# Kernel optimization log

Measured on AMD Instinct MI355X. Metric: run time of the kernel, lower is better.

Reference implementation:

```python
import jax, jax.numpy as jnp
from jax import lax
import numpy as np

ALPHA = 1.702  # GLU sigmoid scale
LIMIT = 7.0    # swiglu_limit


def _moe_forward(hidden_states, topk_weights, topk_ids, gate_up_proj, gate_up_proj_bias, down_proj, down_proj_bias):
    T, H = hidden_states.shape
    E = gate_up_proj.shape[0]
    K = topk_ids.shape[1]
    flat = jnp.ravel(topk_ids)                               # [T*K]
    sorted_sel = jnp.argsort(flat, stable=True)              # dispatch permutation
    sorted_token = sorted_sel // K                           # source token per slot
    sorted_inputs = jnp.take(hidden_states, sorted_token, axis=0)  # [T*K, H]
    expert_ids = jnp.take(flat, sorted_sel, axis=0)          # [T*K]
    group_sizes = jnp.bincount(flat, length=E).astype(jnp.int32)
    # grouped GEMM 1: [T*K,H] x [E,H,2F] -> [T*K,2F]
    gate_up = lax.ragged_dot(sorted_inputs, gate_up_proj, group_sizes)
    gate_up = gate_up + gate_up_proj_bias[expert_ids]
    gate = jnp.minimum(gate_up[..., ::2], LIMIT)
    up = jnp.clip(gate_up[..., 1::2], -LIMIT, LIMIT)
    glu = gate * jax.nn.sigmoid(gate * ALPHA)
    intermediate = (up + 1.0) * glu                          # [T*K, F]
    # grouped GEMM 2: [T*K,F] x [E,F,H] -> [T*K,H]
    out = lax.ragged_dot(intermediate, down_proj, group_sizes)
    out = out + down_proj_bias[expert_ids]
    unsort = jnp.argsort(sorted_sel, stable=True)
    out = jnp.take(out, unsort, axis=0).reshape(T, K, H).astype(jnp.float32)
    combined = jnp.einsum('tkh,tk->th', out, topk_weights.astype(jnp.float32))
    return combined.astype(hidden_states.dtype)


def setup_inputs() -> dict:
    key = jax.random.key(0)
    ks = jax.random.split(key, 7)
    T, H, E, F, K = 16384, 1024, 16, 2048, 2
    scale = 0.02
    hidden_states = jax.random.normal(ks[0], (T, H), jnp.float32)
    w = jax.random.uniform(ks[1], (T, K), jnp.float32) + 1e-3
    topk_weights = w / jnp.sum(w, axis=-1, keepdims=True)
    topk_ids = jax.random.randint(ks[2], (T, K), 0, E, dtype=jnp.int32)
    gate_up_proj = jax.random.normal(ks[3], (E, H, 2 * F), jnp.float32) * scale
    gate_up_proj_bias = jax.random.normal(ks[4], (E, 2 * F), jnp.float32) * scale
    down_proj = jax.random.normal(ks[5], (E, F, H), jnp.float32) * scale
    down_proj_bias = jax.random.normal(ks[6], (E, H), jnp.float32) * scale
    return {"hidden_states": hidden_states, "topk_weights": topk_weights, "topk_ids": topk_ids,
            "gate_up_proj": gate_up_proj, "gate_up_proj_bias": gate_up_proj_bias,
            "down_proj": down_proj, "down_proj_bias": down_proj_bias}


def reference(hidden_states, topk_weights, topk_ids, gate_up_proj, gate_up_proj_bias, down_proj, down_proj_bias):
    return _moe_forward(hidden_states, topk_weights, topk_ids, gate_up_proj, gate_up_proj_bias, down_proj, down_proj_bias)
```

## Files before the change

### kernel.cpp

```cpp
#include <hip/hip_runtime.h>
#include <hip/hip_bf16.h>

typedef unsigned short ushort_t;
typedef __attribute__((ext_vector_type(8))) short bf16x8;
typedef __attribute__((ext_vector_type(4))) float f32x4;

#define T_TOK 16384
#define H_DIM 1024
#define E_NUM 16
#define F_DIM 2048
#define TK    32768
#define MAX_TILES 272

static __device__ __forceinline__ unsigned short f2bf(float f) {
    unsigned int u = __builtin_bit_cast(unsigned int, f);
    unsigned int r = (u + 0x7fffu + ((u >> 16) & 1u)) >> 16;
    return (unsigned short)r;
}

#define GLOAD_LDS16(gp, lp) \
    __builtin_amdgcn_global_load_lds( \
        (const __attribute__((address_space(1))) unsigned int*)(gp), \
        (__attribute__((address_space(3))) unsigned int*)(lp), 16, 0, 0)

__global__ void k_hist(const int* __restrict__ ids, int* __restrict__ meta) {
    __shared__ int h[E_NUM];
    int tid = threadIdx.x;
    if (tid < E_NUM) h[tid] = 0;
    __syncthreads();
    int i = blockIdx.x * 256 + tid;
    atomicAdd(&h[ids[i]], 1);
    __syncthreads();
    if (tid < E_NUM) atomicAdd(&meta[tid], h[tid]);
}

__global__ void k_scan(int* __restrict__ meta) {
    if (threadIdx.x != 0) return;
    int off = 0;
    for (int e = 0; e < E_NUM; ++e) {
        meta[16 + e] = off;
        meta[40 + e] = off;
        off += meta[e];
    }
    meta[32] = off;
    int nt = 0;
    for (int e = 0; e < E_NUM; ++e) {
        int s = meta[16 + e], en = s + meta[e];
        for (int r = s; r < en; r += 128) {
            meta[128 + nt * 3 + 0] = r;
            meta[128 + nt * 3 + 1] = en;
            meta[128 + nt * 3 + 2] = e;
            ++nt;
        }
    }
    meta[64] = nt;
}

__global__ void k_scatter(const int* __restrict__ ids, int* __restrict__ meta,
                          int* __restrict__ row2slot, int* __restrict__ pos2slot) {
    int i = blockIdx.x * 256 + threadIdx.x;
    int e = ids[i];
    int p = atomicAdd(&meta[40 + e], 1);
    row2slot[p] = i;
    pos2slot[i] = p;
}

__global__ void k_gather(const float* __restrict__ hs, const int* __restrict__ row2slot,
                         ushort_t* __restrict__ A1) {
    int r = blockIdx.x;
    int tid = threadIdx.x;
    int tok = row2slot[r] >> 1;
    float4 v = *(const float4*)(hs + (size_t)tok * H_DIM + tid * 4);
    ushort4 o;
    o.x = f2bf(v.x); o.y = f2bf(v.y); o.z = f2bf(v.z); o.w = f2bf(v.w);
    *(ushort4*)(A1 + (size_t)r * H_DIM + tid * 4) = o;
}

__global__ void k_w1conv(const float* __restrict__ gu, ushort_t* __restrict__ w1g,
                         ushort_t* __restrict__ w1u) {
    __shared__ float t[64][65];
    int b = blockIdx.x;
    int nt = b & 63;
    int kt = (b >> 6) & 15;
    int e  = b >> 10;
    int n0 = nt * 64, k0 = kt * 64;
    const float* src = gu + ((size_t)e * H_DIM + k0) * (2 * F_DIM) + n0;
    for (int i = threadIdx.x; i < 64 * 64; i += 256) {
        int kr = i >> 6, nc = i & 63;
        t[kr][nc] = src[(size_t)kr * (2 * F_DIM) + nc];
    }
    __syncthreads();
    ushort_t* dg = w1g + ((size_t)e * F_DIM + (n0 >> 1)) * H_DIM + k0;
    ushort_t* du = w1u + ((size_t)e * F_DIM + (n0 >> 1)) * H_DIM + k0;
    for (int i = threadIdx.x; i < 32 * 64; i += 256) {
        int jl = i >> 6, kc = i & 63;
        dg[(size_t)jl * H_DIM + kc] = f2bf(t[kc][2 * jl]);
        du[(size_t)jl * H_DIM + kc] = f2bf(t[kc][2 * jl + 1]);
    }
}

__global__ void k_w2conv(const float* __restrict__ dp, ushort_t* __restrict__ w2t) {
    __shared__ float t[64][65];
    int b = blockIdx.x;
    int ht = b & 15;
    int ft = (b >> 4) & 31;
    int e  = b >> 9;
    int h0 = ht * 64, f0 = ft * 64;
    const float* src = dp + ((size_t)e * F_DIM + f0) * H_DIM + h0;
    for (int i = threadIdx.x; i < 64 * 64; i += 256) {
        int fr = i >> 6, hc = i & 63;
        t[fr][hc] = src[(size_t)fr * H_DIM + hc];
    }
    __syncthreads();
    ushort_t* d = w2t + ((size_t)e * H_DIM + h0) * F_DIM + f0;
    for (int i = threadIdx.x; i < 64 * 64; i += 256) {
        int hl = i >> 6, fc = i & 63;
        d[(size_t)hl * F_DIM + fc] = f2bf(t[fc][hl]);
    }
}

__global__ __launch_bounds__(256) void k_gemm1(
    const ushort_t* __restrict__ A1, const ushort_t* __restrict__ W1g,
    const ushort_t* __restrict__ W1u, const float* __restrict__ bias,
    ushort_t* __restrict__ inter, const int* __restrict__ meta) {
    int nt = meta[64];
    int slot = blockIdx.y;
    if (slot >= nt) return;
    int row0    = meta[128 + slot * 3 + 0];
    int row_end = meta[128 + slot * 3 + 1];
    int e       = meta[128 + slot * 3 + 2];
    int j0 = blockIdx.x * 64;
    int tid = threadIdx.x, lane = tid & 63, wid = tid >> 6;
    int wm = wid & 1, wj = wid >> 1;
    int lm = lane & 15, lq = lane >> 4;
    __shared__ char smem[32 * 1024];

    f32x4 accg[4][2], accu[4][2];
#pragma unroll
    for (int mi = 0; mi < 4; ++mi)
#pragma unroll
        for (int ji = 0; ji < 2; ++ji) {
            accg[mi][ji] = (f32x4){0.f, 0.f, 0.f, 0.f};
            accu[mi][ji] = (f32x4){0.f, 0.f, 0.f, 0.f};
        }

    for (int kt = 0; kt < 16; ++kt) {
        int kb = kt * 64;
        __syncthreads();
#pragma unroll
        for (int f = 0; f < 8; ++f) {
            int fr = wid * 8 + f;
            const ushort_t* gp;
            if (fr < 16) {
                int mi = fr >> 1, kc = fr & 1;
                int r = row0 + mi * 16 + lm;
                if (r > TK - 1) r = TK - 1;
                gp = A1 + ((size_t)r << 10) + kb + kc * 32 + lq * 8;
            } else if (fr < 24) {
                int g2 = fr - 16; int ji = g2 >> 1, kc = g2 & 1;
                int j = j0 + ji * 16 + lm;
                gp = W1g + (((size_t)(e * F_DIM + j)) << 10) + kb + kc * 32 + lq * 8;
            } else {
                int g2 = fr - 24; int ji = g2 >> 1, kc = g2 & 1;
                int j = j0 + ji * 16 + lm;
                gp = W1u + (((size_t)(e * F_DIM + j)) << 10) + kb + kc * 32 + lq * 8;
            }
            GLOAD_LDS16(gp, smem + fr * 1024);
        }
        __syncthreads();
#pragma unroll
        for (int kc = 0; kc < 2; ++kc) {
            bf16x8 af[4], bg[2], bu[2];
#pragma unroll
            for (int mi = 0; mi < 4; ++mi)
                af[mi] = *(const bf16x8*)(smem + ((wm * 4 + mi) * 2 + kc) * 1024 + lane * 16);
#pragma unroll
            for (int ji = 0; ji < 2; ++ji) {
                bg[ji] = *(const bf16x8*)(smem + 16 * 1024 + ((wj * 2 + ji) * 2 + kc) * 1024 + lane * 16);
                bu[ji] = *(const bf16x8*)(smem + 24 * 1024 + ((wj * 2 + ji) * 2 + kc) * 1024 + lane * 16);
            }
#pragma unroll
            for (int mi = 0; mi < 4; ++mi)
#pragma unroll
                for (int ji = 0; ji < 2; ++ji) {
                    accg[mi][ji] = __builtin_amdgcn_mfma_f32_16x16x32_bf16(af[mi], bg[ji], accg[mi][ji], 0, 0, 0);
                    accu[mi][ji] = __builtin_amdgcn_mfma_f32_16x16x32_bf16(af[mi], bu[ji], accu[mi][ji], 0, 0, 0);
                }
        }
    }
#pragma unroll
    for (int mi = 0; mi < 4; ++mi)
#pragma unroll
        for (int ji = 0; ji < 2; ++ji) {
            int j = j0 + (wj * 2 + ji) * 16 + lm;
            float bgv = bias[e * (2 * F_DIM) + 2 * j];
            float buv = bias[e * (2 * F_DIM) + 2 * j + 1];
#pragma unroll
            for (int r = 0; r < 4; ++r) {
                int row = row0 + wm * 64 + mi * 16 + lq * 4 + r;
                if (row < row_end) {
                    float g = accg[mi][ji][r] + bgv;
                    g = fminf(g, 7.0f);
                    float u = accu[mi][ji][r] + buv;
                    u = fminf(fmaxf(u, -7.0f), 7.0f);
                    float glu = g / (1.0f + __expf(-1.702f * g));
                    inter[((size_t)row << 11) + j] = f2bf((u + 1.0f) * glu);
                }
            }
        }
}

__global__ __launch_bounds__(256) void k_gemm2(
    const ushort_t* __restrict__ Ain, const ushort_t* __restrict__ W2t,
    float* __restrict__ out2, const int* __restrict__ meta) {
    int nt = meta[64];
    int slot = blockIdx.y;
    if (slot >= nt) return;
    int row0    = meta[128 + slot * 3 + 0];
    int row_end = meta[128 + slot * 3 + 1];
    int e       = meta[128 + slot * 3 + 2];
    int n0 = blockIdx.x * 128;
    int tid = threadIdx.x, lane = tid & 63, wid = tid >> 6;
    int wm = wid & 1, wn = wid >> 1;
    int lm = lane & 15, lq = lane >> 4;
    __shared__ char smem[32 * 1024];

    f32x4 acc[4][4];
#pragma unroll
    for (int mi = 0; mi < 4; ++mi)
#pragma unroll
        for (int ni = 0; ni < 4; ++ni) acc[mi][ni] = (f32x4){0.f, 0.f, 0.f, 0.f};

    for (int kt = 0; kt < 32; ++kt) {
        int kb = kt * 64;
        __syncthreads();
#pragma unroll
        for (int f = 0; f < 8; ++f) {
            int fr = wid * 8 + f;
            const ushort_t* gp;
            if (fr < 16) {
                int mi = fr >> 1, kc = fr & 1;
                int r = row0 + mi * 16 + lm;
                if (r > TK - 1) r = TK - 1;
                gp = Ain + ((size_t)r << 11) + kb + kc * 32 + lq * 8;
            } else {
                int g2 = fr - 16; int ni = g2 >> 1, kc = g2 & 1;
                int n = n0 + ni * 16 + lm;
                gp = W2t + (((size_t)(e * H_DIM + n)) << 11) + kb + kc * 32 + lq * 8;
            }
            GLOAD_LDS16(gp, smem + fr * 1024);
        }
        __syncthreads();
#pragma unroll
        for (int kc = 0; kc < 2; ++kc) {
            bf16x8 af[4], bf[4];
#pragma unroll
            for (int mi = 0; mi < 4; ++mi)
                af[mi] = *(const bf16x8*)(smem + ((wm * 4 + mi) * 2 + kc) * 1024 + lane * 16);
#pragma unroll
            for (int ni = 0; ni < 4; ++ni)
                bf[ni] = *(const bf16x8*)(smem + 16 * 1024 + ((wn * 4 + ni) * 2 + kc) * 1024 + lane * 16);
#pragma unroll
            for (int mi = 0; mi < 4; ++mi)
#pragma unroll
                for (int ni = 0; ni < 4; ++ni)
                    acc[mi][ni] = __builtin_amdgcn_mfma_f32_16x16x32_bf16(af[mi], bf[ni], acc[mi][ni], 0, 0, 0);
        }
    }
#pragma unroll
    for (int mi = 0; mi < 4; ++mi)
#pragma unroll
        for (int ni = 0; ni < 4; ++ni) {
            int n = n0 + (wn * 4 + ni) * 16 + lm;
#pragma unroll
            for (int r = 0; r < 4; ++r) {
                int row = row0 + wm * 64 + mi * 16 + lq * 4 + r;
                if (row < row_end)
                    out2[((size_t)row << 10) + n] = acc[mi][ni][r];
            }
        }
}

__global__ void k_combine(const float* __restrict__ out2, const float* __restrict__ tw,
                          const int* __restrict__ ids, const float* __restrict__ db,
                          const int* __restrict__ pos2slot, float* __restrict__ out) {
    int t = blockIdx.x;
    int tid = threadIdx.x;
    float w0 = tw[2 * t], w1 = tw[2 * t + 1];
    int p0 = pos2slot[2 * t], p1 = pos2slot[2 * t + 1];
    int e0 = ids[2 * t], e1 = ids[2 * t + 1];
    int h = tid * 4;
    float4 a0 = *(const float4*)(out2 + ((size_t)p0 << 10) + h);
    float4 a1 = *(const float4*)(out2 + ((size_t)p1 << 10) + h);
    float4 b0 = *(const float4*)(db + ((size_t)e0 << 10) + h);
    float4 b1 = *(const float4*)(db + ((size_t)e1 << 10) + h);
    float4 o;
    o.x = w0 * (a0.x + b0.x) + w1 * (a1.x + b1.x);
    o.y = w0 * (a0.y + b0.y) + w1 * (a1.y + b1.y);
    o.z = w0 * (a0.z + b0.z) + w1 * (a1.z + b1.z);
    o.w = w0 * (a0.w + b0.w) + w1 * (a1.w + b1.w);
    *(float4*)(out + (size_t)t * H_DIM + h) = o;
}

#define WS_META      0
#define WS_R2S       8192
#define WS_P2S       139264
#define WS_A1        270336
#define WS_W1G       67379200
#define WS_W1U       134488064
#define WS_W2T       201596928
#define WS_INTER     268705792

extern "C" void kernel_launch(void* const* d_in, const int* in_sizes, int n_in,
                              void* d_out, int out_size, void* d_ws, size_t ws_size,
                              hipStream_t stream) {
    (void)in_sizes; (void)n_in; (void)out_size; (void)ws_size;
    const float* hs  = (const float*)d_in[0];
    const float* tw  = (const float*)d_in[1];
    const int*   ids = (const int*)d_in[2];
    const float* gup = (const float*)d_in[3];
    const float* gub = (const float*)d_in[4];
    const float* dp  = (const float*)d_in[5];
    const float* dpb = (const float*)d_in[6];
    float* out = (float*)d_out;
    char* ws = (char*)d_ws;

    int* meta          = (int*)(ws + WS_META);
    int* row2slot      = (int*)(ws + WS_R2S);
    int* pos2slot      = (int*)(ws + WS_P2S);
    ushort_t* A1       = (ushort_t*)(ws + WS_A1);
    ushort_t* W1g      = (ushort_t*)(ws + WS_W1G);
    ushort_t* W1u      = (ushort_t*)(ws + WS_W1U);
    ushort_t* W2t      = (ushort_t*)(ws + WS_W2T);
    ushort_t* inter    = (ushort_t*)(ws + WS_INTER);
    float* out2        = (float*)(ws + WS_W1G);

    hipMemsetAsync(meta, 0, 8192, stream);
    k_hist<<<128, 256, 0, stream>>>(ids, meta);
    k_scan<<<1, 64, 0, stream>>>(meta);
    k_scatter<<<128, 256, 0, stream>>>(ids, meta, row2slot, pos2slot);
    k_gather<<<TK, 256, 0, stream>>>(hs, row2slot, A1);
    k_w1conv<<<16384, 256, 0, stream>>>(gup, W1g, W1u);
    k_w2conv<<<8192, 256, 0, stream>>>(dp, W2t);
    k_gemm1<<<dim3(32, MAX_TILES), 256, 0, stream>>>(A1, W1g, W1u, gub, inter, meta);
    k_gemm2<<<dim3(8, MAX_TILES), 256, 0, stream>>>(inter, W2t, out2, meta);
    k_combine<<<T_TOK, 256, 0, stream>>>(out2, tw, ids, dpb, pos2slot, out);
}
```

Before: 1.621 ms.

## Double-buffer LDS tiles in both grouped GEMM kernels to overlap loads with MFMA

```diff
diff --git a/kernel.cpp b/kernel.cpp
--- a/kernel.cpp
+++ b/kernel.cpp
@@ -133,7 +133,35 @@
     int tid = threadIdx.x, lane = tid & 63, wid = tid >> 6;
     int wm = wid & 1, wj = wid >> 1;
     int lm = lane & 15, lq = lane >> 4;
-    __shared__ char smem[32 * 1024];
+    __shared__ char smem[2][32 * 1024];
+
+    const ushort_t* gbase[8];
+#pragma unroll
+    for (int f = 0; f < 8; ++f) {
+        int fr = wid * 8 + f;
+        const ushort_t* gp;
+        if (fr < 16) {
+            int mi = fr >> 1, kc = fr & 1;
+            int r = row0 + mi * 16 + lm;
+            if (r > TK - 1) r = TK - 1;
+            gp = A1 + ((size_t)r << 10) + kc * 32 + lq * 8;
+        } else if (fr < 24) {
+            int g2 = fr - 16; int ji = g2 >> 1, kc = g2 & 1;
+            int j = j0 + ji * 16 + lm;
+            gp = W1g + (((size_t)(e * F_DIM + j)) << 10) + kc * 32 + lq * 8;
+        } else {
+            int g2 = fr - 24; int ji = g2 >> 1, kc = g2 & 1;
+            int j = j0 + ji * 16 + lm;
+            gp = W1u + (((size_t)(e * F_DIM + j)) << 10) + kc * 32 + lq * 8;
+        }
+        gbase[f] = gp;
+    }
+
+    auto stage = [&](int buf, int kb) {
+#pragma unroll
+        for (int f = 0; f < 8; ++f)
+            GLOAD_LDS16(gbase[f] + kb, smem[buf] + (wid * 8 + f) * 1024);
+    };
 
     f32x4 accg[4][2], accu[4][2];
 #pragma unroll
@@ -144,40 +172,23 @@
             accu[mi][ji] = (f32x4){0.f, 0.f, 0.f, 0.f};
         }
 
+    stage(0, 0);
+    __syncthreads();
+
     for (int kt = 0; kt < 16; ++kt) {
-        int kb = kt * 64;
-        __syncthreads();
-#pragma unroll
-        for (int f = 0; f < 8; ++f) {
-            int fr = wid * 8 + f;
-            const ushort_t* gp;
-            if (fr < 16) {
-                int mi = fr >> 1, kc = fr & 1;
-                int r = row0 + mi * 16 + lm;
-                if (r > TK - 1) r = TK - 1;
-                gp = A1 + ((size_t)r << 10) + kb + kc * 32 + lq * 8;
-            } else if (fr < 24) {
-                int g2 = fr - 16; int ji = g2 >> 1, kc = g2 & 1;
-                int j = j0 + ji * 16 + lm;
-                gp = W1g + (((size_t)(e * F_DIM + j)) << 10) + kb + kc * 32 + lq * 8;
-            } else {
-                int g2 = fr - 24; int ji = g2 >> 1, kc = g2 & 1;
-                int j = j0 + ji * 16 + lm;
-                gp = W1u + (((size_t)(e * F_DIM + j)) << 10) + kb + kc * 32 + lq * 8;
-            }
-            GLOAD_LDS16(gp, smem + fr * 1024);
-        }
-        __syncthreads();
+        int cb = kt & 1;
+        if (kt < 15) stage(cb ^ 1, (kt + 1) * 64);
+        const char* base = smem[cb];
 #pragma unroll
         for (int kc = 0; kc < 2; ++kc) {
             bf16x8 af[4], bg[2], bu[2];
 #pragma unroll
             for (int mi = 0; mi < 4; ++mi)
-                af[mi] = *(const bf16x8*)(smem + ((wm * 4 + mi) * 2 + kc) * 1024 + lane * 16);
+                af[mi] = *(const bf16x8*)(base + ((wm * 4 + mi) * 2 + kc) * 1024 + lane * 16);
 #pragma unroll
             for (int ji = 0; ji < 2; ++ji) {
-                bg[ji] = *(const bf16x8*)(smem + 16 * 1024 + ((wj * 2 + ji) * 2 + kc) * 1024 + lane * 16);
-                bu[ji] = *(const bf16x8*)(smem + 24 * 1024 + ((wj * 2 + ji) * 2 + kc) * 1024 + lane * 16);
+                bg[ji] = *(const bf16x8*)(base + 16 * 1024 + ((wj * 2 + ji) * 2 + kc) * 1024 + lane * 16);
+                bu[ji] = *(const bf16x8*)(base + 24 * 1024 + ((wj * 2 + ji) * 2 + kc) * 1024 + lane * 16);
             }
 #pragma unroll
             for (int mi = 0; mi < 4; ++mi)
@@ -187,7 +198,9 @@
                     accu[mi][ji] = __builtin_amdgcn_mfma_f32_16x16x32_bf16(af[mi], bu[ji], accu[mi][ji], 0, 0, 0);
                 }
         }
-    }
+        __syncthreads();
+    }
+
 #pragma unroll
     for (int mi = 0; mi < 4; ++mi)
 #pragma unroll
@@ -223,7 +236,31 @@
     int tid = threadIdx.x, lane = tid & 63, wid = tid >> 6;
     int wm = wid & 1, wn = wid >> 1;
     int lm = lane & 15, lq = lane >> 4;
-    __shared__ char smem[32 * 1024];
+    __shared__ char smem[2][32 * 1024];
+
+    const ushort_t* gbase[8];
+#pragma unroll
+    for (int f = 0; f < 8; ++f) {
+        int fr = wid * 8 + f;
+        const ushort_t* gp;
+        if (fr < 16) {
+            int mi = fr >> 1, kc = fr & 1;
+            int r = row0 + mi * 16 + lm;
+            if (r > TK - 1) r = TK - 1;
+            gp = Ain + ((size_t)r << 11) + kc * 32 + lq * 8;
+        } else {
+            int g2 = fr - 16; int ni = g2 >> 1, kc = g2 & 1;
+            int n = n0 + ni * 16 + lm;
+            gp = W2t + (((size_t)(e * H_DIM + n)) << 11) + kc * 32 + lq * 8;
+        }
+        gbase[f] = gp;
+    }
+
+    auto stage = [&](int buf, int kb) {
+#pragma unroll
+        for (int f = 0; f < 8; ++f)
+            GLOAD_LDS16(gbase[f] + kb, smem[buf] + (wid * 8 + f) * 1024);
+    };
 
     f32x4 acc[4][4];
 #pragma unroll
@@ -231,41 +268,29 @@
 #pragma unroll
         for (int ni = 0; ni < 4; ++ni) acc[mi][ni] = (f32x4){0.f, 0.f, 0.f, 0.f};
 
+    stage(0, 0);
+    __syncthreads();
+
     for (int kt = 0; kt < 32; ++kt) {
-        int kb = kt * 64;
+        int cb = kt & 1;
+        if (kt < 31) stage(cb ^ 1, (kt + 1) * 64);
+        const char* base = smem[cb];
+#pragma unroll
+        for (int kc = 0; kc < 2; ++kc) {
+            bf16x8 af[4], bfr[4];
+#pragma unroll
+            for (int mi = 0; mi < 4; ++mi)
+                af[mi] = *(const bf16x8*)(base + ((wm * 4 + mi) * 2 + kc) * 1024 + lane * 16);
+#pragma unroll
+            for (int ni = 0; ni < 4; ++ni)
+                bfr[ni] = *(const bf16x8*)(base + 16 * 1024 + ((wn * 4 + ni) * 2 + kc) * 1024 + lane * 16);
+#pragma unroll
+            for (int mi = 0; mi < 4; ++mi)
+#pragma unroll
+                for (int ni = 0; ni < 4; ++ni)
+                    acc[mi][ni] = __builtin_amdgcn_mfma_f32_16x16x32_bf16(af[mi], bfr[ni], acc[mi][ni], 0, 0, 0);
+        }
         __syncthreads();
-#pragma unroll
-        for (int f = 0; f < 8; ++f) {
-            int fr = wid * 8 + f;
-            const ushort_t* gp;
-            if (fr < 16) {
-                int mi = fr >> 1, kc = fr & 1;
-                int r = row0 + mi * 16 + lm;
-                if (r > TK - 1) r = TK - 1;
-                gp = Ain + ((size_t)r << 11) + kb + kc * 32 + lq * 8;
-            } else {
-                int g2 = fr - 16; int ni = g2 >> 1, kc = g2 & 1;
-                int n = n0 + ni * 16 + lm;
-                gp = W2t + (((size_t)(e * H_DIM + n)) << 11) + kb + kc * 32 + lq * 8;
-            }
-            GLOAD_LDS16(gp, smem + fr * 1024);
-        }
-        __syncthreads();
-#pragma unroll
-        for (int kc = 0; kc < 2; ++kc) {
-            bf16x8 af[4], bf[4];
-#pragma unroll
-            for (int mi = 0; mi < 4; ++mi)
-                af[mi] = *(const bf16x8*)(smem + ((wm * 4 + mi) * 2 + kc) * 1024 + lane * 16);
-#pragma unroll
-            for (int ni = 0; ni < 4; ++ni)
-                bf[ni] = *(const bf16x8*)(smem + 16 * 1024 + ((wn * 4 + ni) * 2 + kc) * 1024 + lane * 16);
-#pragma unroll
-            for (int mi = 0; mi < 4; ++mi)
-#pragma unroll
-                for (int ni = 0; ni < 4; ++ni)
-                    acc[mi][ni] = __builtin_amdgcn_mfma_f32_16x16x32_bf16(af[mi], bf[ni], acc[mi][ni], 0, 0, 0);
-        }
     }
 #pragma unroll
     for (int mi = 0; mi < 4; ++mi)
```

Result: no change. 1.611 ms (-0.6%).

## Use 256-row tiles with 512 threads and triple-buffered async LDS pipeline in grouped GEMMs

Applied to the files above, without the earlier changes.

```diff
diff --git a/kernel.cpp b/kernel.cpp
--- a/kernel.cpp
+++ b/kernel.cpp
@@ -10,7 +10,7 @@
 #define E_NUM 16
 #define F_DIM 2048
 #define TK    32768
-#define MAX_TILES 272
+#define MAX_TILES 160
 
 static __device__ __forceinline__ unsigned short f2bf(float f) {
     unsigned int u = __builtin_bit_cast(unsigned int, f);
@@ -22,6 +22,10 @@
     __builtin_amdgcn_global_load_lds( \
         (const __attribute__((address_space(1))) unsigned int*)(gp), \
         (__attribute__((address_space(3))) unsigned int*)(lp), 16, 0, 0)
+
+#define SBAR()    asm volatile("s_barrier" ::: "memory")
+#define WAIT_VM6() asm volatile("s_waitcnt vmcnt(6)" ::: "memory")
+#define WAIT_VM0() asm volatile("s_waitcnt vmcnt(0)" ::: "memory")
 
 __global__ void k_hist(const int* __restrict__ ids, int* __restrict__ meta) {
     __shared__ int h[E_NUM];
@@ -46,7 +50,7 @@
     int nt = 0;
     for (int e = 0; e < E_NUM; ++e) {
         int s = meta[16 + e], en = s + meta[e];
-        for (int r = s; r < en; r += 128) {
+        for (int r = s; r < en; r += 256) {
             meta[128 + nt * 3 + 0] = r;
             meta[128 + nt * 3 + 1] = en;
             meta[128 + nt * 3 + 2] = e;
@@ -119,7 +123,7 @@
     }
 }
 
-__global__ __launch_bounds__(256) void k_gemm1(
+__global__ __launch_bounds__(512) void k_gemm1(
     const ushort_t* __restrict__ A1, const ushort_t* __restrict__ W1g,
     const ushort_t* __restrict__ W1u, const float* __restrict__ bias,
     ushort_t* __restrict__ inter, const int* __restrict__ meta) {
@@ -133,84 +137,111 @@
     int tid = threadIdx.x, lane = tid & 63, wid = tid >> 6;
     int wm = wid & 1, wj = wid >> 1;
     int lm = lane & 15, lq = lane >> 4;
-    __shared__ char smem[32 * 1024];
-
-    f32x4 accg[4][2], accu[4][2];
-#pragma unroll
-    for (int mi = 0; mi < 4; ++mi)
-#pragma unroll
-        for (int ji = 0; ji < 2; ++ji) {
-            accg[mi][ji] = (f32x4){0.f, 0.f, 0.f, 0.f};
-            accu[mi][ji] = (f32x4){0.f, 0.f, 0.f, 0.f};
-        }
-
-    for (int kt = 0; kt < 16; ++kt) {
-        int kb = kt * 64;
-        __syncthreads();
-#pragma unroll
-        for (int f = 0; f < 8; ++f) {
-            int fr = wid * 8 + f;
-            const ushort_t* gp;
-            if (fr < 16) {
-                int mi = fr >> 1, kc = fr & 1;
-                int r = row0 + mi * 16 + lm;
-                if (r > TK - 1) r = TK - 1;
-                gp = A1 + ((size_t)r << 10) + kb + kc * 32 + lq * 8;
-            } else if (fr < 24) {
-                int g2 = fr - 16; int ji = g2 >> 1, kc = g2 & 1;
-                int j = j0 + ji * 16 + lm;
-                gp = W1g + (((size_t)(e * F_DIM + j)) << 10) + kb + kc * 32 + lq * 8;
-            } else {
-                int g2 = fr - 24; int ji = g2 >> 1, kc = g2 & 1;
-                int j = j0 + ji * 16 + lm;
-                gp = W1u + (((size_t)(e * F_DIM + j)) << 10) + kb + kc * 32 + lq * 8;
-            }
-            GLOAD_LDS16(gp, smem + fr * 1024);
-        }
-        __syncthreads();
-#pragma unroll
-        for (int kc = 0; kc < 2; ++kc) {
-            bf16x8 af[4], bg[2], bu[2];
-#pragma unroll
-            for (int mi = 0; mi < 4; ++mi)
-                af[mi] = *(const bf16x8*)(smem + ((wm * 4 + mi) * 2 + kc) * 1024 + lane * 16);
-#pragma unroll
-            for (int ji = 0; ji < 2; ++ji) {
-                bg[ji] = *(const bf16x8*)(smem + 16 * 1024 + ((wj * 2 + ji) * 2 + kc) * 1024 + lane * 16);
-                bu[ji] = *(const bf16x8*)(smem + 24 * 1024 + ((wj * 2 + ji) * 2 + kc) * 1024 + lane * 16);
-            }
-#pragma unroll
-            for (int mi = 0; mi < 4; ++mi)
-#pragma unroll
-                for (int ji = 0; ji < 2; ++ji) {
-                    accg[mi][ji] = __builtin_amdgcn_mfma_f32_16x16x32_bf16(af[mi], bg[ji], accg[mi][ji], 0, 0, 0);
-                    accu[mi][ji] = __builtin_amdgcn_mfma_f32_16x16x32_bf16(af[mi], bu[ji], accu[mi][ji], 0, 0, 0);
+    __shared__ char smem[3][48 * 1024];
+
+    const ushort_t* gbase[6];
+    int ldsoff[6];
+#pragma unroll
+    for (int i = 0; i < 6; ++i) {
+        int f = wid * 6 + i;
+        if (f < 32) {
+            int mb = f >> 1, kc = f & 1;
+            int r = row0 + mb * 16 + lm;
+            if (r > TK - 1) r = TK - 1;
+            gbase[i] = A1 + ((size_t)r << 10) + kc * 32 + lq * 8;
+            ldsoff[i] = f * 1024;
+        } else if (f < 40) {
+            int q = f - 32; int jj = q >> 1, kc = q & 1;
+            int j = j0 + jj * 16 + lm;
+            gbase[i] = W1g + (((size_t)(e * F_DIM + j)) << 10) + kc * 32 + lq * 8;
+            ldsoff[i] = 32768 + q * 1024;
+        } else {
+            int q = f - 40; int jj = q >> 1, kc = q & 1;
+            int j = j0 + jj * 16 + lm;
+            gbase[i] = W1u + (((size_t)(e * F_DIM + j)) << 10) + kc * 32 + lq * 8;
+            ldsoff[i] = 40960 + q * 1024;
+        }
+    }
+
+    f32x4 accg[8], accu[8];
+#pragma unroll
+    for (int mi = 0; mi < 8; ++mi) {
+        accg[mi] = (f32x4){0.f, 0.f, 0.f, 0.f};
+        accu[mi] = (f32x4){0.f, 0.f, 0.f, 0.f};
+    }
+
+    char* b0 = (char*)smem;
+    char* b1 = b0 + 49152;
+    char* b2 = b0 + 98304;
+#pragma unroll
+    for (int i = 0; i < 6; ++i) GLOAD_LDS16(gbase[i], b0 + ldsoff[i]);
+#pragma unroll
+    for (int i = 0; i < 6; ++i) GLOAD_LDS16(gbase[i] + 64, b1 + ldsoff[i]);
+
+    for (int t = 0; t < 16; ++t) {
+        if (t == 15) { WAIT_VM0(); } else { WAIT_VM6(); }
+        SBAR();
+        bool st = (t < 14);
+        int kb2 = (t + 2) * 64;
+        bf16x8 bg[2], bu[2];
+#pragma unroll
+        for (int p = 0; p < 4; ++p) {
+            bf16x8 af[2][2];
+#pragma unroll
+            for (int m2 = 0; m2 < 2; ++m2)
+#pragma unroll
+                for (int kc = 0; kc < 2; ++kc)
+                    af[m2][kc] = *(const bf16x8*)(b0 + ((wm * 8 + p * 2 + m2) * 2 + kc) * 1024 + lane * 16);
+            if (p == 0) {
+#pragma unroll
+                for (int kc = 0; kc < 2; ++kc) {
+                    bg[kc] = *(const bf16x8*)(b0 + 32768 + (wj * 2 + kc) * 1024 + lane * 16);
+                    bu[kc] = *(const bf16x8*)(b0 + 40960 + (wj * 2 + kc) * 1024 + lane * 16);
                 }
-        }
-    }
-#pragma unroll
-    for (int mi = 0; mi < 4; ++mi)
-#pragma unroll
-        for (int ji = 0; ji < 2; ++ji) {
-            int j = j0 + (wj * 2 + ji) * 16 + lm;
-            float bgv = bias[e * (2 * F_DIM) + 2 * j];
-            float buv = bias[e * (2 * F_DIM) + 2 * j + 1];
-#pragma unroll
-            for (int r = 0; r < 4; ++r) {
-                int row = row0 + wm * 64 + mi * 16 + lq * 4 + r;
-                if (row < row_end) {
-                    float g = accg[mi][ji][r] + bgv;
-                    g = fminf(g, 7.0f);
-                    float u = accu[mi][ji][r] + buv;
-                    u = fminf(fmaxf(u, -7.0f), 7.0f);
-                    float glu = g / (1.0f + __expf(-1.702f * g));
-                    inter[((size_t)row << 11) + j] = f2bf((u + 1.0f) * glu);
+            }
+            if (st) {
+                if (p == 0)      { GLOAD_LDS16(gbase[0] + kb2, b2 + ldsoff[0]);
+                                   GLOAD_LDS16(gbase[1] + kb2, b2 + ldsoff[1]); }
+                else if (p == 1) { GLOAD_LDS16(gbase[2] + kb2, b2 + ldsoff[2]);
+                                   GLOAD_LDS16(gbase[3] + kb2, b2 + ldsoff[3]); }
+                else if (p == 2) { GLOAD_LDS16(gbase[4] + kb2, b2 + ldsoff[4]); }
+                else             { GLOAD_LDS16(gbase[5] + kb2, b2 + ldsoff[5]); }
+            }
+            __builtin_amdgcn_s_setprio(1);
+#pragma unroll
+            for (int m2 = 0; m2 < 2; ++m2)
+#pragma unroll
+                for (int kc = 0; kc < 2; ++kc) {
+                    accg[p * 2 + m2] = __builtin_amdgcn_mfma_f32_16x16x32_bf16(af[m2][kc], bg[kc], accg[p * 2 + m2], 0, 0, 0);
+                    accu[p * 2 + m2] = __builtin_amdgcn_mfma_f32_16x16x32_bf16(af[m2][kc], bu[kc], accu[p * 2 + m2], 0, 0, 0);
                 }
-            }
-        }
-}
-
-__global__ __launch_bounds__(256) void k_gemm2(
+            __builtin_amdgcn_s_setprio(0);
+            SBAR();
+        }
+        char* tmp = b0; b0 = b1; b1 = b2; b2 = tmp;
+    }
+
+    int j = j0 + wj * 16 + lm;
+    float bgv = bias[e * (2 * F_DIM) + 2 * j];
+    float buv = bias[e * (2 * F_DIM) + 2 * j + 1];
+#pragma unroll
+    for (int mi = 0; mi < 8; ++mi) {
+#pragma unroll
+        for (int r = 0; r < 4; ++r) {
+            int row = row0 + wm * 128 + mi * 16 + lq * 4 + r;
+            if (row < row_end) {
+                float g = accg[mi][r] + bgv;
+                g = fminf(g, 7.0f);
+                float u = accu[mi][r] + buv;
+                u = fminf(fmaxf(u, -7.0f), 7.0f);
+                float glu = g / (1.0f + __expf(-1.702f * g));
+                inter[((size_t)row << 11) + j] = f2bf((u + 1.0f) * glu);
+            }
+        }
+    }
+}
+
+__global__ __launch_bounds__(512) void k_gemm2(
     const ushort_t* __restrict__ Ain, const ushort_t* __restrict__ W2t,
     float* __restrict__ out2, const int* __restrict__ meta) {
     int nt = meta[64];
@@ -223,58 +254,92 @@
     int tid = threadIdx.x, lane = tid & 63, wid = tid >> 6;
     int wm = wid & 1, wn = wid >> 1;
     int lm = lane & 15, lq = lane >> 4;
-    __shared__ char smem[32 * 1024];
-
-    f32x4 acc[4][4];
-#pragma unroll
-    for (int mi = 0; mi < 4; ++mi)
-#pragma unroll
-        for (int ni = 0; ni < 4; ++ni) acc[mi][ni] = (f32x4){0.f, 0.f, 0.f, 0.f};
-
-    for (int kt = 0; kt < 32; ++kt) {
-        int kb = kt * 64;
-        __syncthreads();
-#pragma unroll
-        for (int f = 0; f < 8; ++f) {
-            int fr = wid * 8 + f;
-            const ushort_t* gp;
-            if (fr < 16) {
-                int mi = fr >> 1, kc = fr & 1;
-                int r = row0 + mi * 16 + lm;
-                if (r > TK - 1) r = TK - 1;
-                gp = Ain + ((size_t)r << 11) + kb + kc * 32 + lq * 8;
-            } else {
-                int g2 = fr - 16; int ni = g2 >> 1, kc = g2 & 1;
-                int n = n0 + ni * 16 + lm;
-                gp = W2t + (((size_t)(e * H_DIM + n)) << 11) + kb + kc * 32 + lq * 8;
-            }
-            GLOAD_LDS16(gp, smem + fr * 1024);
-        }
-        __syncthreads();
-#pragma unroll
-        for (int kc = 0; kc < 2; ++kc) {
-            bf16x8 af[4], bf[4];
-#pragma unroll
-            for (int mi = 0; mi < 4; ++mi)
-                af[mi] = *(const bf16x8*)(smem + ((wm * 4 + mi) * 2 + kc) * 1024 + lane * 16);
-#pragma unroll
-            for (int ni = 0; ni < 4; ++ni)
-                bf[ni] = *(const bf16x8*)(smem + 16 * 1024 + ((wn * 4 + ni) * 2 + kc) * 1024 + lane * 16);
-#pragma unroll
-            for (int mi = 0; mi < 4; ++mi)
-#pragma unroll
-                for (int ni = 0; ni < 4; ++ni)
-                    acc[mi][ni] = __builtin_amdgcn_mfma_f32_16x16x32_bf16(af[mi], bf[ni], acc[mi][ni], 0, 0, 0);
-        }
-    }
-#pragma unroll
-    for (int mi = 0; mi < 4; ++mi)
-#pragma unroll
-        for (int ni = 0; ni < 4; ++ni) {
-            int n = n0 + (wn * 4 + ni) * 16 + lm;
+    __shared__ char smem[3][48 * 1024];
+
+    const ushort_t* gbase[6];
+    int ldsoff[6];
+#pragma unroll
+    for (int i = 0; i < 6; ++i) {
+        int f = wid * 6 + i;
+        if (f < 32) {
+            int mb = f >> 1, kc = f & 1;
+            int r = row0 + mb * 16 + lm;
+            if (r > TK - 1) r = TK - 1;
+            gbase[i] = Ain + ((size_t)r << 11) + kc * 32 + lq * 8;
+            ldsoff[i] = f * 1024;
+        } else {
+            int q = f - 32; int nb = q >> 1, kc = q & 1;
+            int n = n0 + nb * 16 + lm;
+            gbase[i] = W2t + (((size_t)(e * H_DIM + n)) << 11) + kc * 32 + lq * 8;
+            ldsoff[i] = 32768 + q * 1024;
+        }
+    }
+
+    f32x4 acc[8][2];
+#pragma unroll
+    for (int mi = 0; mi < 8; ++mi)
+#pragma unroll
+        for (int ni = 0; ni < 2; ++ni) acc[mi][ni] = (f32x4){0.f, 0.f, 0.f, 0.f};
+
+    char* b0 = (char*)smem;
+    char* b1 = b0 + 49152;
+    char* b2 = b0 + 98304;
+#pragma unroll
+    for (int i = 0; i < 6; ++i) GLOAD_LDS16(gbase[i], b0 + ldsoff[i]);
+#pragma unroll
+    for (int i = 0; i < 6; ++i) GLOAD_LDS16(gbase[i] + 64, b1 + ldsoff[i]);
+
+    for (int t = 0; t < 32; ++t) {
+        if (t == 31) { WAIT_VM0(); } else { WAIT_VM6(); }
+        SBAR();
+        bool st = (t < 30);
+        int kb2 = (t + 2) * 64;
+        bf16x8 bb[2][2];
+#pragma unroll
+        for (int p = 0; p < 4; ++p) {
+            bf16x8 af[2][2];
+#pragma unroll
+            for (int m2 = 0; m2 < 2; ++m2)
+#pragma unroll
+                for (int kc = 0; kc < 2; ++kc)
+                    af[m2][kc] = *(const bf16x8*)(b0 + ((wm * 8 + p * 2 + m2) * 2 + kc) * 1024 + lane * 16);
+            if (p == 0) {
+#pragma unroll
+                for (int ni = 0; ni < 2; ++ni)
+#pragma unroll
+                    for (int kc = 0; kc < 2; ++kc)
+                        bb[ni][kc] = *(const bf16x8*)(b0 + 32768 + ((wn * 2 + ni) * 2 + kc) * 1024 + lane * 16);
+            }
+            if (st) {
+                if (p == 0)      { GLOAD_LDS16(gbase[0] + kb2, b2 + ldsoff[0]);
+                                   GLOAD_LDS16(gbase[1] + kb2, b2 + ldsoff[1]); }
+                else if (p == 1) { GLOAD_LDS16(gbase[2] + kb2, b2 + ldsoff[2]);
+                                   GLOAD_LDS16(gbase[3] + kb2, b2 + ldsoff[3]); }
+                else if (p == 2) { GLOAD_LDS16(gbase[4] + kb2, b2 + ldsoff[4]); }
+                else             { GLOAD_LDS16(gbase[5] + kb2, b2 + ldsoff[5]); }
+            }
+            __builtin_amdgcn_s_setprio(1);
+#pragma unroll
+            for (int m2 = 0; m2 < 2; ++m2)
+#pragma unroll
+                for (int ni = 0; ni < 2; ++ni)
+#pragma unroll
+                    for (int kc = 0; kc < 2; ++kc)
+                        acc[p * 2 + m2][ni] = __builtin_amdgcn_mfma_f32_16x16x32_bf16(af[m2][kc], bb[ni][kc], acc[p * 2 + m2][ni], 0, 0, 0);
+            __builtin_amdgcn_s_setprio(0);
+            SBAR();
+        }
+        char* tmp = b0; b0 = b1; b1 = b2; b2 = tmp;
+    }
+
+#pragma unroll
+    for (int mi = 0; mi < 8; ++mi)
+#pragma unroll
+        for (int ni = 0; ni < 2; ++ni) {
+            int n = n0 + (wn * 2 + ni) * 16 + lm;
 #pragma unroll
             for (int r = 0; r < 4; ++r) {
-                int row = row0 + wm * 64 + mi * 16 + lq * 4 + r;
+                int row = row0 + wm * 128 + mi * 16 + lq * 4 + r;
                 if (row < row_end)
                     out2[((size_t)row << 10) + n] = acc[mi][ni][r];
             }
@@ -342,7 +407,7 @@
     k_gather<<<TK, 256, 0, stream>>>(hs, row2slot, A1);
     k_w1conv<<<16384, 256, 0, stream>>>(gup, W1g, W1u);
     k_w2conv<<<8192, 256, 0, stream>>>(dp, W2t);
-    k_gemm1<<<dim3(32, MAX_TILES), 256, 0, stream>>>(A1, W1g, W1u, gub, inter, meta);
-    k_gemm2<<<dim3(8, MAX_TILES), 256, 0, stream>>>(inter, W2t, out2, meta);
+    k_gemm1<<<dim3(32, MAX_TILES), 512, 0, stream>>>(A1, W1g, W1u, gub, inter, meta);
+    k_gemm2<<<dim3(8, MAX_TILES), 512, 0, stream>>>(inter, W2t, out2, meta);
     k_combine<<<T_TOK, 256, 0, stream>>>(out2, tw, ids, dpb, pos2slot, out);
 }
```

After: 1.462 ms. -9.8%, faster.
